# Kernel tuning notes

Measured on AMD Instinct MI355X. Metric: run time of the kernel, lower is better.

The kernel has to match this reference:

```python
import jax, jax.numpy as jnp
import numpy as np

BATCH, LENGTH, HIDDEN, SSM = 32, 2048, 128, 256


def setup_inputs() -> dict:
    key = jax.random.key(0)
    ks = jax.random.split(key, 7)
    b_std = 1.0 / np.sqrt(HIDDEN)
    c_std = 1.0 / np.sqrt(SSM)
    return {
        "inputs": jax.random.normal(ks[0], (BATCH, LENGTH, HIDDEN), jnp.float32),
        "A_diag": jax.random.normal(ks[1], (SSM,), jnp.float32),
        "G_diag": jax.random.uniform(ks[2], (SSM,), jnp.float32),
        "steps": jax.random.normal(ks[3], (SSM,), jnp.float32) * 0.5,
        "B": jax.random.uniform(ks[4], (SSM, HIDDEN, 2), jnp.float32, -b_std, b_std),
        "C": jax.random.uniform(ks[5], (HIDDEN, SSM, 2), jnp.float32, -c_std, c_std),
        "D": jax.random.normal(ks[6], (HIDDEN,), jnp.float32),
    }


def _project_parameters(A_diag, G_diag, steps):
    # Mirrors DampedLinOSSLayer._project_parameters: sigmoid step, relu damping,
    # and clamp A into the band where the 2x2 IMEX1 transition has complex eigenvalues.
    step = jax.nn.sigmoid(steps)
    g = jax.nn.relu(G_diag)
    denom = jnp.maximum(step * step, 1e-6)
    s = step * g
    base = jnp.sqrt(jnp.maximum(1.0 + s, 1e-6))
    a_low = (2.0 + s - 2.0 * base) / denom
    a_high = (2.0 + s + 2.0 * base) / denom
    a = a_low + jax.nn.relu(A_diag - a_low) - jax.nn.relu(A_diag - a_high)
    return a, g, step


def _eigenvalue(a, g, step):
    # IMEX1 transition M = [[S, -S*dt*A], [dt*S, 1 - dt^2*S*A]] with S = 1/(1+dt*G).
    # det(M) = S, trace(M) = S + 1 - dt^2*S*A; projection guarantees trace^2 < 4*det,
    # so eigenvalues form a conjugate pair lam = T/2 + i*sqrt(S - T^2/4).
    S = 1.0 / (1.0 + step * g)
    T = S + 1.0 - step * step * S * a
    imag = jnp.sqrt(jnp.maximum(S - 0.25 * T * T, 0.0))
    return jax.lax.complex(0.5 * T, imag)  # [P] complex64


def reference(inputs, A_diag, G_diag, steps, B, C, D):
    a, g, step = _project_parameters(A_diag, G_diag, steps)
    lam = _eigenvalue(a, g, step)  # [P]

    # Complex input projection: bu = (B_re + i*B_im) @ u, shape [batch, L, P]
    bu = jax.lax.complex(
        jnp.einsum("blh,ph->blp", inputs, B[..., 0]),
        jnp.einsum("blh,ph->blp", inputs, B[..., 1]),
    )

    # Diagonal complex linear recurrence x_k = lam * x_{k-1} + bu_k via associative scan.
    def combine(e1, e2):
        a1, b1 = e1
        a2, b2 = e2
        return a1 * a2, a2 * b1 + b2

    lam_b = jnp.broadcast_to(lam[None, None, :], bu.shape)
    _, states = jax.lax.associative_scan(combine, (lam_b, bu), axis=1)

    # Output: Re(C @ x) + D * u
    projected = (
        jnp.einsum("blp,hp->blh", states.real, C[..., 0])
        - jnp.einsum("blp,hp->blh", states.imag, C[..., 1])
    )
    return projected + inputs * D
```

## Files before the change

kernel.cpp:

```cpp
#include <hip/hip_runtime.h>
#include <hip/hip_bf16.h>
#include <math.h>

#define BATCH 32
#define LEN   2048
#define HID   128
#define SSM   256

#define BPL 32768

typedef __attribute__((ext_vector_type(4))) float f32x4;
typedef __attribute__((ext_vector_type(8))) short bf16x8;
typedef __attribute__((ext_vector_type(4))) int   i32x4;

static __device__ __forceinline__ unsigned short f2bf(float x) {
    union { float f; unsigned u; } v; v.f = x;
    unsigned r = (v.u + 0x7FFFu + ((v.u >> 16) & 1u)) >> 16;
    return (unsigned short)r;
}
static __device__ __forceinline__ unsigned short f2bf_hi(float x) {
    union { float f; unsigned u; } v; v.f = x;
    return (unsigned short)(v.u >> 16);
}
static __device__ __forceinline__ float bf2f(unsigned short b) {
    union { unsigned u; float f; } v; v.u = ((unsigned)b) << 16;
    return v.f;
}
static __device__ __forceinline__ unsigned int cvtpk(float a, float b) {
    __hip_bfloat162 h = __float22bfloat162_rn(float2{a, b});
    union { __hip_bfloat162 h2; unsigned int u; } c; c.h2 = h;
    return c.u;
}
static __device__ __forceinline__ void cmul(float& rr, float& ri,
                                            float ar, float ai, float br, float bi) {
    rr = ar * br - ai * bi;
    ri = ar * bi + ai * br;
}
static __device__ __forceinline__ void gload16(const void* g, void* l) {
    __builtin_amdgcn_global_load_lds(
        (const __attribute__((address_space(1))) unsigned int*)g,
        (__attribute__((address_space(3))) unsigned int*)l,
        16, 0, 0);
}

__global__ __launch_bounds__(256) void kprep(const float* __restrict__ u,
                                             const float* __restrict__ Bm,
                                             const float* __restrict__ Cm,
                                             const float* __restrict__ A,
                                             const float* __restrict__ G,
                                             const float* __restrict__ steps,
                                             unsigned short* __restrict__ ubf,
                                             unsigned short* __restrict__ Bsp,
                                             unsigned short* __restrict__ C2,
                                             float* __restrict__ lam) {
    if (blockIdx.x < 2048) {
        const int total = BATCH * LEN * HID;
        const int stride = 2048 * 256 * 8;
        for (int i = (blockIdx.x * 256 + threadIdx.x) * 8; i < total; i += stride) {
            f32x4 a = *(const f32x4*)&u[i];
            f32x4 c = *(const f32x4*)&u[i + 4];
            i32x4 o;
            o[0] = (int)cvtpk(a[0], a[1]);
            o[1] = (int)cvtpk(a[2], a[3]);
            o[2] = (int)cvtpk(c[0], c[1]);
            o[3] = (int)cvtpk(c[2], c[3]);
            *(i32x4*)&ubf[i] = o;
        }
        return;
    }
    if (blockIdx.x == 2304) {
        int p = threadIdx.x;
        if (p < SSM) {
            float stp   = 1.f / (1.f + expf(-steps[p]));
            float g     = fmaxf(G[p], 0.f);
            float denom = fmaxf(stp * stp, 1e-6f);
            float s     = stp * g;
            float base  = sqrtf(fmaxf(1.f + s, 1e-6f));
            float alow  = (2.f + s - 2.f * base) / denom;
            float ahigh = (2.f + s + 2.f * base) / denom;
            float a     = alow + fmaxf(A[p] - alow, 0.f) - fmaxf(A[p] - ahigh, 0.f);
            float S     = 1.f / (1.f + stp * g);
            float T     = S + 1.f - stp * stp * S * a;
            lam[p]       = 0.5f * T;
            lam[SSM + p] = sqrtf(fmaxf(S - 0.25f * T * T, 0.f));
        }
        return;
    }
    int gidx = (blockIdx.x - 2048) * 256 + threadIdx.x;
    if (gidx < 32768) {
        int p = gidx >> 7, h = gidx & 127;
        float vr = Bm[(size_t)(p * HID + h) * 2];
        float vi = Bm[(size_t)(p * HID + h) * 2 + 1];
        unsigned short hh = f2bf_hi(vr);
        Bsp[0 * BPL + p * HID + h] = hh;
        Bsp[1 * BPL + p * HID + h] = f2bf(vr - bf2f(hh));
        hh = f2bf_hi(vi);
        Bsp[2 * BPL + p * HID + h] = hh;
        Bsp[3 * BPL + p * HID + h] = f2bf(vi - bf2f(hh));
    } else {
        int g2 = gidx - 32768;
        int h = g2 >> 8, p = g2 & 255;
        float vr = Cm[(size_t)(h * SSM + p) * 2];
        float vi = -Cm[(size_t)(h * SSM + p) * 2 + 1];
        unsigned short rh = f2bf_hi(vr);
        unsigned short ih = f2bf_hi(vi);
        size_t rowh = (size_t)h * 512;
        C2[rowh + 2 * p]               = rh;
        C2[rowh + 2 * p + 1]           = ih;
        C2[65536 + rowh + 2 * p]       = f2bf(vr - bf2f(rh));
        C2[65536 + rowh + 2 * p + 1]   = f2bf(vi - bf2f(ih));
    }
}

__global__ __launch_bounds__(512, 4) void k12_fused(const unsigned short* __restrict__ ubf,
                                                    const unsigned short* __restrict__ Bsp,
                                                    const float* __restrict__ lam,
                                                    unsigned short* __restrict__ TP) {
    __shared__ __align__(16) char sU[2][32768];
    __shared__ float Rld[2][4][2][8][2];

    int d    = blockIdx.x;
    int xcd  = d & 7;
    int idx  = d >> 3;
    int pt   = idx & 15;
    int bhi  = idx >> 4;
    int b    = bhi * 8 + xcd;
    int p0   = pt * 16;

    int tid  = threadIdx.x;
    int lane = tid & 63, w = tid >> 6;
    int wl   = w >> 1, wp = w & 1;
    int fr   = lane & 15, g = lane >> 4;
    int frp  = fr & 7;
    int comp = fr >> 3;
    int pcol = p0 + wp * 8 + frp;

    const unsigned short* Bh  = Bsp + (size_t)(comp * 2) * BPL + (size_t)pcol * HID;
    const unsigned short* Blo = Bsp + (size_t)(comp * 2 + 1) * BPL + (size_t)pcol * HID;
    bf16x8 Bfh[4], Bfl[4];
#pragma unroll
    for (int kc = 0; kc < 4; ++kc) {
        Bfh[kc] = *(const bf16x8*)&Bh[kc * 32 + g * 8];
        Bfl[kc] = *(const bf16x8*)&Blo[kc * 32 + g * 8];
    }

    float pw_r[4], pw_i[4];
    float lg_r, lg_i;
    float l4r, l4i, l8r, l8i, l16r, l16i, l32r, l32i;
    {
        float ar = lam[pcol], ai = lam[SSM + pcol];
        pw_r[0] = ar; pw_i[0] = ai;
        cmul(pw_r[1], pw_i[1], ar, ai, ar, ai);
        cmul(pw_r[2], pw_i[2], pw_r[1], pw_i[1], ar, ai);
        cmul(pw_r[3], pw_i[3], pw_r[1], pw_i[1], pw_r[1], pw_i[1]);
        l4r = pw_r[3]; l4i = pw_i[3];
        cmul(l8r, l8i, l4r, l4i, l4r, l4i);
        cmul(l16r, l16i, l8r, l8i, l8r, l8i);
        cmul(l32r, l32i, l16r, l16i, l16r, l16i);
        if (g == 0)      { lg_r = 1.f; lg_i = 0.f; }
        else if (g == 1) { lg_r = l4r; lg_i = l4i; }
        else if (g == 2) { lg_r = l8r; lg_i = l8i; }
        else             { cmul(lg_r, lg_i, l8r, l8i, l4r, l4i); }
    }

    float TCr = 0.f, TCi = 0.f;

    const unsigned short* ub = ubf + (size_t)b * (LEN * HID);
    int srow32  = tid >> 4;
    int stg_src = srow32 * HID + ((((tid & 15) * 16) ^ ((srow32 & 7) << 4)) >> 1);

#define STAGE(buf, tt)                                                        \
    {                                                                         \
        const unsigned short* gs = ub + (size_t)(tt) * 16384 + stg_src;       \
        char* ls = &sU[buf][tid * 16];                                        \
        _Pragma("unroll")                                                     \
        for (int q = 0; q < 4; ++q)                                           \
            gload16(gs + q * 4096, ls + q * 8192);                            \
    }

    STAGE(0, 0)
    __syncthreads();
    int cur = 0;

    int colb = wl * 32 + comp * 16 + g * 4;

    for (int t = 0; t < 16; ++t) {
        int l0t = t * 128;

        if (t < 15) STAGE(cur ^ 1, t + 1)

        const char* su = &sU[cur][0];
        f32x4 accA[2], accB[2];
        accA[0] = (f32x4)(0.f); accA[1] = (f32x4)(0.f);
        accB[0] = (f32x4)(0.f); accB[1] = (f32x4)(0.f);
#pragma unroll
        for (int kc = 0; kc < 2; ++kc) {
#pragma unroll
            for (int mi = 0; mi < 2; ++mi) {
                int off0 = (wl * 32 + mi * 16 + fr) * 256 + ((kc * 64 + g * 16) ^ ((fr & 7) << 4));
                int off1 = (wl * 32 + mi * 16 + fr) * 256 + (((kc + 2) * 64 + g * 16) ^ ((fr & 7) << 4));
                bf16x8 ah0 = *(const bf16x8*)(su + off0);
                bf16x8 ah1 = *(const bf16x8*)(su + off1);
                accA[mi] = __builtin_amdgcn_mfma_f32_16x16x32_bf16(ah0, Bfh[kc], accA[mi], 0, 0, 0);
                accA[mi] = __builtin_amdgcn_mfma_f32_16x16x32_bf16(ah0, Bfl[kc], accA[mi], 0, 0, 0);
                accB[mi] = __builtin_amdgcn_mfma_f32_16x16x32_bf16(ah1, Bfh[kc + 2], accB[mi], 0, 0, 0);
                accB[mi] = __builtin_amdgcn_mfma_f32_16x16x32_bf16(ah1, Bfl[kc + 2], accB[mi], 0, 0, 0);
            }
        }
        f32x4 acc[2];
        acc[0] = accA[0] + accB[0];
        acc[1] = accA[1] + accB[1];

        float xr[4], xi[4];
#pragma unroll
        for (int e = 0; e < 4; ++e) {
            float send = (comp == 0) ? acc[1][e] : acc[0][e];
            float oth  = __shfl_xor(send, 8, 64);
            xr[e] = (comp == 0) ? acc[0][e] : oth;
            xi[e] = (comp == 0) ? oth       : acc[1][e];
        }

        float Er, Ei, Fr, Fi, For, Foi;
        {
            float lr = pw_r[0], li = pw_i[0];
            float cr = 0.f, ci = 0.f;
#pragma unroll
            for (int r = 0; r < 4; ++r) {
                float nr = fmaf(lr, cr, fmaf(-li, ci, xr[r]));
                float ni = fmaf(lr, ci, fmaf(li, cr, xi[r]));
                cr = nr; ci = ni;
                xr[r] = cr; xi[r] = ci;
            }
            float Qr = cr, Qi = ci;
            float ur = __shfl_up(Qr, 16u, 64);
            float ui = __shfl_up(Qi, 16u, 64);
            if (g >= 1) {
                Qr = fmaf(l4r, ur, fmaf(-l4i, ui, Qr));
                Qi = fmaf(l4r, ui, fmaf(l4i, ur, Qi));
            }
            ur = __shfl_up(Qr, 32u, 64);
            ui = __shfl_up(Qi, 32u, 64);
            if (g >= 2) {
                Qr = fmaf(l8r, ur, fmaf(-l8i, ui, Qr));
                Qi = fmaf(l8r, ui, fmaf(l8i, ur, Qi));
            }
            Er = __shfl_up(Qr, 16u, 64);
            Ei = __shfl_up(Qi, 16u, 64);
            if (g == 0) { Er = 0.f; Ei = 0.f; }
            Fr = __shfl(Qr, fr + 48, 64);
            Fi = __shfl(Qi, fr + 48, 64);
            For = __shfl_xor(Fr, 8, 64);
            Foi = __shfl_xor(Fi, 8, 64);
            float Rr = fmaf(l16r, For, fmaf(-l16i, Foi, Fr));
            float Ri = fmaf(l16r, Foi, fmaf(l16i, For, Fi));
            if (g == 0 && fr >= 8) { Rld[t & 1][wl][wp][frp][0] = Rr; Rld[t & 1][wl][wp][frp][1] = Ri; }
        }
        __syncthreads();

        {
            float Wr = TCr, Wi = TCi;
            float Tr = TCr, Ti = TCi;
#pragma unroll
            for (int w2 = 0; w2 < 4; ++w2) {
                float rr = Rld[t & 1][w2][wp][frp][0], ri = Rld[t & 1][w2][wp][frp][1];
                float nTr = fmaf(l32r, Tr, fmaf(-l32i, Ti, rr));
                float nTi = fmaf(l32r, Ti, fmaf(l32i, Tr, ri));
                Tr = nTr; Ti = nTi;
                if (w2 < wl) {
                    float nWr = fmaf(l32r, Wr, fmaf(-l32i, Wi, rr));
                    float nWi = fmaf(l32r, Wi, fmaf(l32i, Wr, ri));
                    Wr = nWr; Wi = nWi;
                }
            }
            TCr = Tr; TCi = Ti;
            float prr, pri;
            if (comp == 0) { prr = Wr; pri = Wi; }
            else {
                prr = fmaf(l16r, Wr, fmaf(-l16i, Wi, For));
                pri = fmaf(l16r, Wi, fmaf(l16i, Wr, Foi));
            }
            float Mr = fmaf(lg_r, prr, fmaf(-lg_i, pri, Er));
            float Mi = fmaf(lg_r, pri, fmaf(lg_i, prr, Ei));
#pragma unroll
            for (int r = 0; r < 4; ++r) {
                xr[r] = fmaf(pw_r[r], Mr, fmaf(-pw_i[r], Mi, xr[r]));
                xi[r] = fmaf(pw_r[r], Mi, fmaf(pw_i[r], Mr, xi[r]));
            }
        }

        {
            size_t rowbase = ((size_t)(b * LEN) + l0t + colb) * 512 + pcol * 2;
#pragma unroll
            for (int r = 0; r < 4; ++r)
                *(unsigned int*)&TP[rowbase + (size_t)r * 512] = cvtpk(xr[r], xi[r]);
        }
        cur ^= 1;
    }
#undef STAGE
}

__global__ __launch_bounds__(512, 4) void k3_out(const unsigned short* __restrict__ TP,
                                                 const unsigned short* __restrict__ C2,
                                                 const unsigned short* __restrict__ ubf,
                                                 const float* __restrict__ D,
                                                 float* __restrict__ out) {
    __shared__ __align__(16) char sAB[3][24576];

    int d    = blockIdx.x;
    int xcd  = d & 7;
    int rest = d >> 3;
    int lt   = rest & 15;
    int bhi  = rest >> 4;
    int b    = bhi * 8 + xcd;
    int l0   = lt * 128;

    int tid = threadIdx.x;
    int lane = tid & 63, w = tid >> 6;
    int wl = w >> 1, wh = w & 1;
    int fr = lane & 15, g = lane >> 4;

    f32x4 acc[2][4];
#pragma unroll
    for (int mi = 0; mi < 2; ++mi)
#pragma unroll
        for (int ni = 0; ni < 4; ++ni) acc[mi][ni] = (f32x4)(0.f);

    float dv[4];
#pragma unroll
    for (int ni = 0; ni < 4; ++ni) dv[ni] = D[wh * 64 + ni * 16 + fr];

#define STAGE3(buf, cc)                                                       \
    {                                                                         \
        {                                                                     \
            int rw = tid >> 2, sl = tid & 3;                                  \
            gload16(TP + ((size_t)(b * LEN) + l0 + rw) * 512 + (cc) * 32 +    \
                        ((sl ^ (rw & 3)) * 8),                                \
                    &sAB[buf][tid * 16]);                                     \
        }                                                                     \
        _Pragma("unroll")                                                     \
        for (int q = 0; q < 2; ++q) {                                         \
            int dg = tid + q * 512;                                           \
            int hl = dg >> 9, hr = (dg >> 2) & 127, sl = dg & 3;              \
            gload16(C2 + ((size_t)(hl * 128 + hr)) * 512 + (cc) * 32 +        \
                        ((sl ^ (hr & 3)) * 8),                                \
                    &sAB[buf][8192 + dg * 16]);                               \
        }                                                                     \
    }

    STAGE3(0, 0)
    __syncthreads();
    STAGE3(1, 1)

    int cur = 0;
    for (int c = 0; c < 16; ++c) {
        if (c < 14) STAGE3((cur + 2) % 3, c + 2)

        const char* sb = &sAB[cur][0];
        int swz = (g ^ (fr & 3)) * 16;
        bf16x8 af[2];
#pragma unroll
        for (int mi = 0; mi < 2; ++mi) {
            int arow = wl * 32 + mi * 16 + fr;
            af[mi] = *(const bf16x8*)(sb + arow * 64 + swz);
        }
#pragma unroll
        for (int ni = 0; ni < 4; ++ni) {
            int hrow = wh * 64 + ni * 16 + fr;
            bf16x8 ch = *(const bf16x8*)(sb + 8192 + hrow * 64 + swz);
            bf16x8 cl = *(const bf16x8*)(sb + 8192 + 8192 + hrow * 64 + swz);
#pragma unroll
            for (int mi = 0; mi < 2; ++mi) {
                acc[mi][ni] = __builtin_amdgcn_mfma_f32_16x16x32_bf16(af[mi], ch, acc[mi][ni], 0, 0, 0);
                acc[mi][ni] = __builtin_amdgcn_mfma_f32_16x16x32_bf16(af[mi], cl, acc[mi][ni], 0, 0, 0);
            }
        }
        if (c < 14) {
            asm volatile("s_waitcnt vmcnt(3) lgkmcnt(0)" ::: "memory");
        } else {
            asm volatile("s_waitcnt vmcnt(0) lgkmcnt(0)" ::: "memory");
        }
        __builtin_amdgcn_s_barrier();
        __builtin_amdgcn_sched_barrier(0);
        cur = (cur + 1) % 3;
    }
#undef STAGE3

#pragma unroll
    for (int mi = 0; mi < 2; ++mi)
#pragma unroll
        for (int ni = 0; ni < 4; ++ni) {
            int lb = l0 + wl * 32 + mi * 16 + g * 4;
            int h  = wh * 64 + ni * 16 + fr;
#pragma unroll
            for (int r = 0; r < 4; ++r) {
                size_t idx = ((size_t)b * LEN + lb + r) * HID + h;
                out[idx] = acc[mi][ni][r] + bf2f(ubf[idx]) * dv[ni];
            }
        }
}

extern "C" void kernel_launch(void* const* d_in, const int* in_sizes, int n_in,
                              void* d_out, int out_size, void* d_ws, size_t ws_size,
                              hipStream_t stream) {
    const float* u  = (const float*)d_in[0];
    const float* A  = (const float*)d_in[1];
    const float* G  = (const float*)d_in[2];
    const float* st = (const float*)d_in[3];
    const float* B  = (const float*)d_in[4];
    const float* C  = (const float*)d_in[5];
    const float* D  = (const float*)d_in[6];
    float* out = (float*)d_out;

    char* WS = (char*)d_ws;
    unsigned short* TP  = (unsigned short*)WS;
    float* lam          = (float*)(WS + 67108864);
    unsigned short* Bsp = (unsigned short*)(WS + 67110912);
    unsigned short* C2  = (unsigned short*)(WS + 67373056);
    unsigned short* ubf = (unsigned short*)(WS + 67635200);

    kprep<<<2305, 256, 0, stream>>>(u, B, C, A, G, st, ubf, Bsp, C2, lam);
    k12_fused<<<512, 512, 0, stream>>>(ubf, Bsp, lam, TP);
    k3_out<<<512, 512, 0, stream>>>(TP, C2, ubf, D, out);
}
```

Before: 79.31 us.

## Software-pipeline scan kernel: prefetch two tiles ahead and overlap GEMM with carry fixup

Restructures the chunked scan loop so the MFMA projection for tile t+1 is issued before the cross-wave carry fixup and store of tile t, with global staging moved two tiles ahead. The intra-chunk scan phase for the next tile runs after the current tile's output write, and MFMA sections are wrapped in s_setprio to favour matrix issue. This aims to hide LDS/global latency and the barrier bubble behind MFMA work, at the cost of more live registers (accumulators plus xr/xi across phases), which may hurt occupancy under the existing launch bounds.

Result: no change. 79.23 us (-0.1%).

```diff
diff --git a/kernel.cpp b/kernel.cpp
--- a/kernel.cpp
+++ b/kernel.cpp
@@ -178,84 +178,94 @@
             gload16(gs + q * 4096, ls + q * 8192);                            \
     }
 
+    float xr[4], xi[4];
+    float Er, Ei, For, Foi;
+
+#define DO_GEMM(bufidx)                                                       \
+    {                                                                         \
+        const char* su = &sU[bufidx][0];                                      \
+        accA[0] = (f32x4)(0.f); accA[1] = (f32x4)(0.f);                       \
+        accB[0] = (f32x4)(0.f); accB[1] = (f32x4)(0.f);                       \
+        __builtin_amdgcn_s_setprio(1);                                        \
+        _Pragma("unroll")                                                     \
+        for (int kc = 0; kc < 2; ++kc) {                                      \
+            _Pragma("unroll")                                                 \
+            for (int mi = 0; mi < 2; ++mi) {                                  \
+                int off0 = (wl * 32 + mi * 16 + fr) * 256 +                   \
+                           ((kc * 64 + g * 16) ^ ((fr & 7) << 4));            \
+                int off1 = (wl * 32 + mi * 16 + fr) * 256 +                   \
+                           (((kc + 2) * 64 + g * 16) ^ ((fr & 7) << 4));      \
+                bf16x8 ah0 = *(const bf16x8*)(su + off0);                     \
+                bf16x8 ah1 = *(const bf16x8*)(su + off1);                     \
+                accA[mi] = __builtin_amdgcn_mfma_f32_16x16x32_bf16(ah0, Bfh[kc], accA[mi], 0, 0, 0);     \
+                accA[mi] = __builtin_amdgcn_mfma_f32_16x16x32_bf16(ah0, Bfl[kc], accA[mi], 0, 0, 0);     \
+                accB[mi] = __builtin_amdgcn_mfma_f32_16x16x32_bf16(ah1, Bfh[kc + 2], accB[mi], 0, 0, 0); \
+                accB[mi] = __builtin_amdgcn_mfma_f32_16x16x32_bf16(ah1, Bfl[kc + 2], accB[mi], 0, 0, 0); \
+            }                                                                 \
+        }                                                                     \
+        __builtin_amdgcn_s_setprio(0);                                        \
+    }
+
+#define DO_PH1(rb)                                                            \
+    {                                                                         \
+        f32x4 acc0 = accA[0] + accB[0];                                       \
+        f32x4 acc1 = accA[1] + accB[1];                                       \
+        _Pragma("unroll")                                                     \
+        for (int e = 0; e < 4; ++e) {                                         \
+            float send = (comp == 0) ? acc1[e] : acc0[e];                     \
+            float oth  = __shfl_xor(send, 8, 64);                             \
+            xr[e] = (comp == 0) ? acc0[e] : oth;                              \
+            xi[e] = (comp == 0) ? oth     : acc1[e];                          \
+        }                                                                     \
+        float lr = pw_r[0], li = pw_i[0];                                     \
+        float cr = 0.f, ci = 0.f;                                             \
+        _Pragma("unroll")                                                     \
+        for (int r = 0; r < 4; ++r) {                                         \
+            float nr = fmaf(lr, cr, fmaf(-li, ci, xr[r]));                    \
+            float ni = fmaf(lr, ci, fmaf(li, cr, xi[r]));                     \
+            cr = nr; ci = ni;                                                 \
+            xr[r] = cr; xi[r] = ci;                                           \
+        }                                                                     \
+        float Qr = cr, Qi = ci;                                               \
+        float ur = __shfl_up(Qr, 16u, 64);                                    \
+        float ui = __shfl_up(Qi, 16u, 64);                                    \
+        if (g >= 1) {                                                         \
+            Qr = fmaf(l4r, ur, fmaf(-l4i, ui, Qr));                           \
+            Qi = fmaf(l4r, ui, fmaf(l4i, ur, Qi));                            \
+        }                                                                     \
+        ur = __shfl_up(Qr, 32u, 64);                                          \
+        ui = __shfl_up(Qi, 32u, 64);                                          \
+        if (g >= 2) {                                                         \
+            Qr = fmaf(l8r, ur, fmaf(-l8i, ui, Qr));                           \
+            Qi = fmaf(l8r, ui, fmaf(l8i, ur, Qi));                            \
+        }                                                                     \
+        Er = __shfl_up(Qr, 16u, 64);                                          \
+        Ei = __shfl_up(Qi, 16u, 64);                                          \
+        if (g == 0) { Er = 0.f; Ei = 0.f; }                                   \
+        float Fr = __shfl(Qr, fr + 48, 64);                                   \
+        float Fi = __shfl(Qi, fr + 48, 64);                                   \
+        For = __shfl_xor(Fr, 8, 64);                                          \
+        Foi = __shfl_xor(Fi, 8, 64);                                          \
+        float Rr = fmaf(l16r, For, fmaf(-l16i, Foi, Fr));                     \
+        float Ri = fmaf(l16r, Foi, fmaf(l16i, For, Fi));                      \
+        if (g == 0 && fr >= 8) { Rld[rb][wl][wp][frp][0] = Rr; Rld[rb][wl][wp][frp][1] = Ri; } \
+    }
+
+    int colb = wl * 32 + comp * 16 + g * 4;
+    f32x4 accA[2], accB[2];
+
     STAGE(0, 0)
     __syncthreads();
-    int cur = 0;
-
-    int colb = wl * 32 + comp * 16 + g * 4;
+    STAGE(1, 1)
+    DO_GEMM(0)
+    DO_PH1(0)
+    __syncthreads();
 
     for (int t = 0; t < 16; ++t) {
         int l0t = t * 128;
 
-        if (t < 15) STAGE(cur ^ 1, t + 1)
-
-        const char* su = &sU[cur][0];
-        f32x4 accA[2], accB[2];
-        accA[0] = (f32x4)(0.f); accA[1] = (f32x4)(0.f);
-        accB[0] = (f32x4)(0.f); accB[1] = (f32x4)(0.f);
-#pragma unroll
-        for (int kc = 0; kc < 2; ++kc) {
-#pragma unroll
-            for (int mi = 0; mi < 2; ++mi) {
-                int off0 = (wl * 32 + mi * 16 + fr) * 256 + ((kc * 64 + g * 16) ^ ((fr & 7) << 4));
-                int off1 = (wl * 32 + mi * 16 + fr) * 256 + (((kc + 2) * 64 + g * 16) ^ ((fr & 7) << 4));
-                bf16x8 ah0 = *(const bf16x8*)(su + off0);
-                bf16x8 ah1 = *(const bf16x8*)(su + off1);
-                accA[mi] = __builtin_amdgcn_mfma_f32_16x16x32_bf16(ah0, Bfh[kc], accA[mi], 0, 0, 0);
-                accA[mi] = __builtin_amdgcn_mfma_f32_16x16x32_bf16(ah0, Bfl[kc], accA[mi], 0, 0, 0);
-                accB[mi] = __builtin_amdgcn_mfma_f32_16x16x32_bf16(ah1, Bfh[kc + 2], accB[mi], 0, 0, 0);
-                accB[mi] = __builtin_amdgcn_mfma_f32_16x16x32_bf16(ah1, Bfl[kc + 2], accB[mi], 0, 0, 0);
-            }
-        }
-        f32x4 acc[2];
-        acc[0] = accA[0] + accB[0];
-        acc[1] = accA[1] + accB[1];
-
-        float xr[4], xi[4];
-#pragma unroll
-        for (int e = 0; e < 4; ++e) {
-            float send = (comp == 0) ? acc[1][e] : acc[0][e];
-            float oth  = __shfl_xor(send, 8, 64);
-            xr[e] = (comp == 0) ? acc[0][e] : oth;
-            xi[e] = (comp == 0) ? oth       : acc[1][e];
-        }
-
-        float Er, Ei, Fr, Fi, For, Foi;
-        {
-            float lr = pw_r[0], li = pw_i[0];
-            float cr = 0.f, ci = 0.f;
-#pragma unroll
-            for (int r = 0; r < 4; ++r) {
-                float nr = fmaf(lr, cr, fmaf(-li, ci, xr[r]));
-                float ni = fmaf(lr, ci, fmaf(li, cr, xi[r]));
-                cr = nr; ci = ni;
-                xr[r] = cr; xi[r] = ci;
-            }
-            float Qr = cr, Qi = ci;
-            float ur = __shfl_up(Qr, 16u, 64);
-            float ui = __shfl_up(Qi, 16u, 64);
-            if (g >= 1) {
-                Qr = fmaf(l4r, ur, fmaf(-l4i, ui, Qr));
-                Qi = fmaf(l4r, ui, fmaf(l4i, ur, Qi));
-            }
-            ur = __shfl_up(Qr, 32u, 64);
-            ui = __shfl_up(Qi, 32u, 64);
-            if (g >= 2) {
-                Qr = fmaf(l8r, ur, fmaf(-l8i, ui, Qr));
-                Qi = fmaf(l8r, ui, fmaf(l8i, ur, Qi));
-            }
-            Er = __shfl_up(Qr, 16u, 64);
-            Ei = __shfl_up(Qi, 16u, 64);
-            if (g == 0) { Er = 0.f; Ei = 0.f; }
-            Fr = __shfl(Qr, fr + 48, 64);
-            Fi = __shfl(Qi, fr + 48, 64);
-            For = __shfl_xor(Fr, 8, 64);
-            Foi = __shfl_xor(Fi, 8, 64);
-            float Rr = fmaf(l16r, For, fmaf(-l16i, Foi, Fr));
-            float Ri = fmaf(l16r, Foi, fmaf(l16i, For, Fi));
-            if (g == 0 && fr >= 8) { Rld[t & 1][wl][wp][frp][0] = Rr; Rld[t & 1][wl][wp][frp][1] = Ri; }
-        }
-        __syncthreads();
+        if (t < 14) STAGE(t & 1, t + 2)
+        if (t < 15) DO_GEMM((t + 1) & 1)
 
         {
             float Wr = TCr, Wi = TCi;
@@ -294,9 +304,14 @@
             for (int r = 0; r < 4; ++r)
                 *(unsigned int*)&TP[rowbase + (size_t)r * 512] = cvtpk(xr[r], xi[r]);
         }
-        cur ^= 1;
+
+        if (t < 15) DO_PH1((t + 1) & 1)
+
+        __syncthreads();
     }
 #undef STAGE
+#undef DO_GEMM
+#undef DO_PH1
 }
 
 __global__ __launch_bounds__(512, 4) void k3_out(const unsigned short* __restrict__ TP,
```
